# Kernel optimization log

Measured on AMD Instinct MI355X. Metric: run time of the kernel, lower is better.

The kernel has to match this reference:

```python
import jax, jax.numpy as jnp
import numpy as np
import math

N, E = 50000, 1600000
IN, HID, OUT, ED, H = 128, 32, 64, 64, 4
HC = H * HID  # 128, input dim of second layer


def setup_inputs() -> dict:
    key = jax.random.key(0)
    ks = jax.random.split(key, 32)
    w = lambda k, shape: (jax.random.normal(k, shape, jnp.float32) * 0.05)
    inp = {
        "x": w(ks[0], (N, IN)),
        "edge_feats": w(ks[1], (E, ED)),
        "edge_index": jax.random.randint(ks[2], (2, E), 0, N, jnp.int32),
        # layer 1: TransformerConv(IN -> HID, heads=H, concat=True, edge_dim=ED)
        "Wq1": w(ks[3], (IN, HC)), "bq1": w(ks[4], (HC,)),
        "Wk1": w(ks[5], (IN, HC)), "bk1": w(ks[6], (HC,)),
        "Wv1": w(ks[7], (IN, HC)), "bv1": w(ks[8], (HC,)),
        "We1": w(ks[9], (ED, HC)),  # lin_edge has no bias in PyG
        "Ws1": w(ks[10], (IN, HC)), "bs1": w(ks[11], (HC,)),
        # layer 2: TransformerConv(HC -> OUT, heads=1, concat=False, edge_dim=ED)
        "Wq2": w(ks[12], (HC, OUT)), "bq2": w(ks[13], (OUT,)),
        "Wk2": w(ks[14], (HC, OUT)), "bk2": w(ks[15], (OUT,)),
        "Wv2": w(ks[16], (HC, OUT)), "bv2": w(ks[17], (OUT,)),
        "We2": w(ks[18], (ED, OUT)),
        "Ws2": w(ks[19], (HC, OUT)), "bs2": w(ks[20], (OUT,)),
    }
    return inp


def tconv(x, src, dst, ef, Wq, bq, Wk, bk, Wv, bv, We, Ws, bs, heads, ch, concat):
    """PyG TransformerConv (beta=False, root_weight=True), eval mode."""
    n = x.shape[0]
    q = (x @ Wq + bq).reshape(n, heads, ch)
    k = (x @ Wk + bk).reshape(n, heads, ch)
    v = (x @ Wv + bv).reshape(n, heads, ch)
    e = (ef @ We).reshape(-1, heads, ch)           # [E,H,C]
    k_j = k[src] + e                                # gather + edge bias
    v_j = v[src] + e
    alpha = jnp.einsum("ehc,ehc->eh", q[dst], k_j) / math.sqrt(ch)  # [E,H]
    # segment softmax over destination nodes
    m = jax.lax.stop_gradient(jax.ops.segment_max(alpha, dst, num_segments=n))
    a = jnp.exp(alpha - m[dst])
    den = jax.ops.segment_sum(a, dst, num_segments=n)
    a = a / den[dst]
    msg = v_j * a[..., None]                        # [E,H,C]
    out = jax.ops.segment_sum(msg, dst, num_segments=n)  # [N,H,C]
    out = out.reshape(n, heads * ch) if concat else out.mean(axis=1)
    return out + x @ Ws + bs                        # root/skip connection


def reference(x, edge_feats, edge_index, Wq1, bq1, Wk1, bk1, Wv1, bv1, We1, Ws1, bs1,
              Wq2, bq2, Wk2, bk2, Wv2, bv2, We2, Ws2, bs2):
    src, dst = edge_index[0], edge_index[1]
    h = tconv(x, src, dst, edge_feats, Wq1, bq1, Wk1, bk1, Wv1, bv1, We1, Ws1, bs1,
              H, HID, True)
    h = jax.nn.relu(h)  # dropout=0.0 (eval) -> identity
    out = tconv(h, src, dst, edge_feats, Wq2, bq2, Wk2, bk2, Wv2, bv2, We2, Ws2, bs2,
                1, OUT, False)
    return out
```

## Files before the change

### kernel.cpp

```cpp
#include <hip/hip_runtime.h>

#define NN 50000
#define EE 1600000

__device__ inline float b2f(unsigned short u) {
    return __uint_as_float(((unsigned)u) << 16);
}
__device__ inline unsigned short f2bf(float f) {
    unsigned u = __float_as_uint(f);
    unsigned r = 0x7fffu + ((u >> 16) & 1u);
    return (unsigned short)((u + r) >> 16);
}
__device__ inline void stv(float* p, size_t i, float v) { p[i] = v; }
__device__ inline void stv(unsigned short* p, size_t i, float v) { p[i] = f2bf(v); }

__global__ void sniff_kernel(const void* w, int* flags) {
    int lane = threadIdx.x;
    const unsigned short* u = (const unsigned short*)w;
    int bad = 0;
    for (int i = lane; i < 256; i += 64) {
        float f = b2f(u[i]);
        if (!(fabsf(f) < 2.0f)) bad++;
    }
    unsigned long long m = __ballot(bad > 0);
    if (lane == 0) {
        flags[0] = (__popcll(m) > 8) ? 1 : 0;
        flags[1] = 0;
    }
}

struct WTab {
    const void* p[18];
    int off[18];
    int sz[18];
};
__global__ void __launch_bounds__(256) convert_kernel(WTab t, const int* __restrict__ flags,
                                                      unsigned short* __restrict__ dst) {
    int f32 = flags[0];
    int ti = blockIdx.y;
    int i = blockIdx.x * 256 + threadIdx.x;
    if (i < t.sz[ti]) {
        dst[t.off[ti] + i] = f32 ? f2bf(((const float*)t.p[ti])[i])
                                 : ((const unsigned short*)t.p[ti])[i];
    }
}

__global__ void __launch_bounds__(256) count_kernel(const int* __restrict__ dst,
                                                    int* __restrict__ cnt) {
    int e = blockIdx.x * 256 + threadIdx.x;
    if (e < EE) atomicAdd(&cnt[dst[e]], 1);
}

__global__ void __launch_bounds__(1024) scan_kernel(int* __restrict__ cntfill,
                                                    int* __restrict__ rowptr) {
    __shared__ int s[1024];
    __shared__ int carry_s;
    int tid = threadIdx.x;
    if (tid == 0) carry_s = 0;
    __syncthreads();
    for (int base = 0; base < NN; base += 4096) {
        int i0 = base + tid * 4;
        int v0 = (i0 + 0 < NN) ? cntfill[i0 + 0] : 0;
        int v1 = (i0 + 1 < NN) ? cntfill[i0 + 1] : 0;
        int v2 = (i0 + 2 < NN) ? cntfill[i0 + 2] : 0;
        int v3 = (i0 + 3 < NN) ? cntfill[i0 + 3] : 0;
        int tsum = v0 + v1 + v2 + v3;
        s[tid] = tsum;
        __syncthreads();
        for (int off = 1; off < 1024; off <<= 1) {
            int t = (tid >= off) ? s[tid - off] : 0;
            __syncthreads();
            s[tid] += t;
            __syncthreads();
        }
        int carry = carry_s;
        int excl = carry + s[tid] - tsum;
        int e0 = excl, e1 = excl + v0, e2 = e1 + v1, e3 = e2 + v2;
        if (i0 + 0 < NN) { rowptr[i0 + 0] = e0; cntfill[i0 + 0] = e0; }
        if (i0 + 1 < NN) { rowptr[i0 + 1] = e1; cntfill[i0 + 1] = e1; }
        if (i0 + 2 < NN) { rowptr[i0 + 2] = e2; cntfill[i0 + 2] = e2; }
        if (i0 + 3 < NN) { rowptr[i0 + 3] = e3; cntfill[i0 + 3] = e3; }
        __syncthreads();
        if (tid == 1023) carry_s = carry + s[1023];
        __syncthreads();
    }
    if (tid == 0) rowptr[NN] = carry_s;
}

__global__ void __launch_bounds__(256) fill_kernel(const int* __restrict__ dst,
                                                   int* __restrict__ cntfill,
                                                   int* __restrict__ perm) {
    int e = blockIdx.x * 256 + threadIdx.x;
    if (e < EE) {
        int p = atomicAdd(&cntfill[dst[e]], 1);
        perm[p] = e;
    }
}

__global__ void __launch_bounds__(256) edge_gather(const int* __restrict__ perm,
                                                   const int* __restrict__ src,
                                                   const void* __restrict__ efp,
                                                   const int* __restrict__ flagp,
                                                   int* __restrict__ src_perm,
                                                   unsigned short* __restrict__ efperm) {
    int ef32 = *flagp;
    int tid = threadIdx.x;
    int j = tid & 15;
    int local = tid >> 4;
    const float* efF = (const float*)efp;
    const unsigned short* efU = (const unsigned short*)efp;
    for (int pass = 0; pass < 4; ++pass) {
        int i = blockIdx.x * 64 + pass * 16 + local;
        if (i < EE) {
            int e = perm[i];
            if (j == 0) src_perm[i] = src[e];
            ushort4 o;
            if (ef32) {
                float4 f = *(const float4*)(efF + (size_t)e * 64 + j * 4);
                o.x = f2bf(f.x); o.y = f2bf(f.y); o.z = f2bf(f.z); o.w = f2bf(f.w);
            } else {
                o = *(const ushort4*)(efU + (size_t)e * 64 + j * 4);
            }
            *(ushort4*)(efperm + (size_t)i * 64 + j * 4) = o;
        }
    }
}

template <typename TO, int K, int OD, int TR, int LAYOUT = 0>
__global__ void __launch_bounds__(256) gemm_node(const void* __restrict__ X,
                                                 const int* __restrict__ flagp,
                                                 const unsigned short* __restrict__ W,
                                                 const unsigned short* __restrict__ bias,
                                                 TO* __restrict__ C, int nrows,
                                                 int ldc, int cstride, int coff) {
    constexpr int TRP = TR + 4;
    __shared__ unsigned short Ws[K * OD];
    __shared__ float Xs[K * TRP];
    int tid = threadIdx.x;
    int xf32 = *flagp;
    for (int i = tid; i < K * OD; i += 256) Ws[i] = W[i];
    int row0 = blockIdx.x * TR;
    const float* Xf = (const float*)X;
    const unsigned short* Xu = (const unsigned short*)X;
    for (int i = tid; i < TR * K; i += 256) {
        int r = i / K, kk = i % K;
        int rr = row0 + r;
        float vv = 0.f;
        if (rr < nrows) {
            size_t idx = (size_t)rr * K + kk;
            vv = xf32 ? Xf[idx] : b2f(Xu[idx]);
        }
        Xs[kk * TRP + r] = vv;
    }
    __syncthreads();
    constexpr int CG = OD / 4;
    int rg = tid / CG, cg = tid % CG;
    int r0 = rg * 4, c0 = cg * 4;
    float acc[4][4] = {};
#pragma unroll 4
    for (int kk = 0; kk < K; ++kk) {
        const float4 xv = *(const float4*)&Xs[kk * TRP + r0];
        ushort4 wu = *(const ushort4*)&Ws[kk * OD + c0];
        float xa[4] = {xv.x, xv.y, xv.z, xv.w};
        float wb[4] = {b2f(wu.x), b2f(wu.y), b2f(wu.z), b2f(wu.w)};
#pragma unroll
        for (int i2 = 0; i2 < 4; i2++)
#pragma unroll
            for (int j2 = 0; j2 < 4; j2++) acc[i2][j2] += xa[i2] * wb[j2];
    }
    float bb[4];
#pragma unroll
    for (int j2 = 0; j2 < 4; j2++) bb[j2] = b2f(bias[c0 + j2]);
#pragma unroll
    for (int i2 = 0; i2 < 4; i2++) {
        int rr = row0 + r0 + i2;
        if (rr < nrows) {
#pragma unroll
            for (int j2 = 0; j2 < 4; j2++) {
                size_t idx;
                if constexpr (LAYOUT == 0) {
                    idx = (size_t)rr * ldc + (size_t)(c0 + j2) * cstride + coff;
                } else {
                    int c = c0 + j2;
                    int hh = c >> 5, r = c & 31;
                    idx = (size_t)rr * 256 +
                          (size_t)((hh * 16 + (r & 15)) * 4 + (r >> 4) +
                                   (LAYOUT == 2 ? 2 : 0));
                }
                stv(C, idx, acc[i2][j2] + bb[j2]);
            }
        }
    }
}

__global__ void __launch_bounds__(256) qe1_kernel(const unsigned short* __restrict__ q,
                                                  const unsigned short* __restrict__ We,
                                                  float* __restrict__ qe) {
    __shared__ float Ws[64 * 129];
    __shared__ float qs[8 * 128];
    int tid = threadIdx.x;
    for (int i = tid; i < 64 * 128; i += 256) Ws[(i / 128) * 129 + (i % 128)] = b2f(We[i]);
    int n0 = blockIdx.x * 8;
    for (int i = tid; i < 8 * 128; i += 256) {
        int n = n0 + (i >> 7);
        qs[i] = (n < NN) ? b2f(q[(size_t)n * 128 + (i & 127)]) : 0.f;
    }
    __syncthreads();
    int h = tid >> 6, d = tid & 63;
    for (int nl = 0; nl < 8; ++nl) {
        int n = n0 + nl;
        if (n < NN) {
            float acc = 0.f;
#pragma unroll
            for (int c = 0; c < 32; ++c)
                acc += qs[nl * 128 + h * 32 + c] * Ws[d * 129 + h * 32 + c];
            qe[(size_t)n * 256 + h * 64 + d] = acc;
        }
    }
}

__global__ void __launch_bounds__(256) qe2_kernel(const unsigned short* __restrict__ q,
                                                  const unsigned short* __restrict__ We,
                                                  float* __restrict__ qe) {
    __shared__ float Ws[64 * 65];
    __shared__ float qs[4 * 64];
    int tid = threadIdx.x;
    for (int i = tid; i < 64 * 64; i += 256) Ws[(i / 64) * 65 + (i % 64)] = b2f(We[i]);
    int n0 = blockIdx.x * 4;
    {
        int n = n0 + (tid >> 6);
        qs[tid] = (n < NN) ? b2f(q[(size_t)n * 64 + (tid & 63)]) : 0.f;
    }
    __syncthreads();
    int nl = tid >> 6, d = tid & 63;
    int n = n0 + nl;
    if (n < NN) {
        float acc = 0.f;
#pragma unroll
        for (int c = 0; c < 64; ++c) acc += qs[nl * 64 + c] * Ws[d * 65 + c];
        qe[(size_t)n * 64 + d] = acc;
    }
}

__device__ __forceinline__ void np1_step(const uint2 (&kvd)[4], const ushort4 (&efd)[4],
                                         float qa, float qb, const float4& qm, float rs,
                                         float& m, float& l, float& a1, float& a2,
                                         float& w0, float& w1, float& w2, float& w3) {
    float t[4];
    float f0[4], f1[4], f2[4], f3[4];
#pragma unroll
    for (int u = 0; u < 4; ++u) {
        float ka = b2f((unsigned short)(kvd[u].x & 0xffffu));
        float kb = b2f((unsigned short)(kvd[u].x >> 16));
        f0[u] = b2f(efd[u].x); f1[u] = b2f(efd[u].y);
        f2[u] = b2f(efd[u].z); f3[u] = b2f(efd[u].w);
        float tt = qa * ka + qb * kb + qm.x * f0[u] + qm.y * f1[u] +
                   qm.z * f2[u] + qm.w * f3[u];
        tt += __shfl_xor(tt, 4);
        tt += __shfl_xor(tt, 8);
        tt += __shfl_xor(tt, 16);
        tt += __shfl_xor(tt, 32);
        t[u] = tt * rs;
    }
    float mn = fmaxf(fmaxf(fmaxf(t[0], t[1]), fmaxf(t[2], t[3])), m);
    float sc = __expf(m - mn);
    float w[4];
#pragma unroll
    for (int u = 0; u < 4; ++u) w[u] = __expf(t[u] - mn);
    m = mn;
    l = l * sc + ((w[0] + w[1]) + (w[2] + w[3]));
    float sa1 = 0.f, sa2 = 0.f, sw0 = 0.f, sw1 = 0.f, sw2 = 0.f, sw3 = 0.f;
#pragma unroll
    for (int u = 0; u < 4; ++u) {
        float va = b2f((unsigned short)(kvd[u].y & 0xffffu));
        float vb = b2f((unsigned short)(kvd[u].y >> 16));
        sa1 += w[u] * va; sa2 += w[u] * vb;
        sw0 += w[u] * f0[u]; sw1 += w[u] * f1[u];
        sw2 += w[u] * f2[u]; sw3 += w[u] * f3[u];
    }
    a1 = a1 * sc + sa1; a2 = a2 * sc + sa2;
    w0 = w0 * sc + sw0; w1 = w1 * sc + sw1;
    w2 = w2 * sc + sw2; w3 = w3 * sc + sw3;
}

__global__ void __launch_bounds__(256) node_pass1(
    const int* __restrict__ rowptr, const int* __restrict__ srcp,
    const unsigned short* __restrict__ q, const unsigned short* __restrict__ kv,
    const float* __restrict__ qe, const unsigned short* __restrict__ efperm,
    float* __restrict__ av, float* __restrict__ wef) {
    int lane = threadIdx.x & 63;
    int node = (blockIdx.x * 256 + threadIdx.x) >> 6;
    if (node >= NN) return;
    int h = lane & 3;
    int dq = lane >> 2;
    int c1 = h * 32 + dq, c2 = c1 + 16;
    int kvoff = (h * 16 + dq) * 4;
    float qa = b2f(q[(size_t)node * 128 + c1]);
    float qb = b2f(q[(size_t)node * 128 + c2]);
    float4 qm = *(const float4*)(qe + (size_t)node * 256 + h * 64 + 4 * dq);
    float m = -__builtin_inff(), l = 0.f, a1 = 0.f, a2 = 0.f;
    float w0 = 0.f, w1 = 0.f, w2 = 0.f, w3 = 0.f;
    int beg = rowptr[node], end = rowptr[node + 1];
    const float rs = 0.17677669529663687f;
    int ng = (end - beg) >> 2;

    int ssA[4], ssB[4];
    uint2 kvA[4], kvB[4];
    ushort4 efA[4], efB[4];

    if (ng > 0) {
#pragma unroll
        for (int u = 0; u < 4; ++u) ssA[u] = srcp[beg + u];
#pragma unroll
        for (int u = 0; u < 4; ++u)
            kvA[u] = *(const uint2*)(kv + (size_t)ssA[u] * 256 + kvoff);
#pragma unroll
        for (int u = 0; u < 4; ++u)
            efA[u] = *(const ushort4*)(efperm + (size_t)(beg + u) * 64 + 4 * dq);
        if (ng > 1) {
#pragma unroll
            for (int u = 0; u < 4; ++u) ssB[u] = srcp[beg + 4 + u];
        }
        int g = 0;
        while (true) {
            bool nextB = (g + 1 < ng);
            if (nextB) {
                int ib = beg + ((g + 1) << 2);
#pragma unroll
                for (int u = 0; u < 4; ++u)
                    kvB[u] = *(const uint2*)(kv + (size_t)ssB[u] * 256 + kvoff);
#pragma unroll
                for (int u = 0; u < 4; ++u)
                    efB[u] = *(const ushort4*)(efperm + (size_t)(ib + u) * 64 + 4 * dq);
                if (g + 2 < ng) {
                    int ib2 = beg + ((g + 2) << 2);
#pragma unroll
                    for (int u = 0; u < 4; ++u) ssA[u] = srcp[ib2 + u];
                }
            }
            np1_step(kvA, efA, qa, qb, qm, rs, m, l, a1, a2, w0, w1, w2, w3);
            if (!nextB) { ++g; break; }
            ++g;
            bool nextA = (g + 1 < ng);
            if (nextA) {
                int ib = beg + ((g + 1) << 2);
#pragma unroll
                for (int u = 0; u < 4; ++u)
                    kvA[u] = *(const uint2*)(kv + (size_t)ssA[u] * 256 + kvoff);
#pragma unroll
                for (int u = 0; u < 4; ++u)
                    efA[u] = *(const ushort4*)(efperm + (size_t)(ib + u) * 64 + 4 * dq);
                if (g + 2 < ng) {
                    int ib2 = beg + ((g + 2) << 2);
#pragma unroll
                    for (int u = 0; u < 4; ++u) ssB[u] = srcp[ib2 + u];
                }
            }
            np1_step(kvB, efB, qa, qb, qm, rs, m, l, a1, a2, w0, w1, w2, w3);
            if (!nextA) { ++g; break; }
            ++g;
        }
    }
    for (int i = beg + (ng << 2); i < end; ++i) {
        int sj = srcp[i];
        uint2 kd = *(const uint2*)(kv + (size_t)sj * 256 + kvoff);
        ushort4 fu = *(const ushort4*)(efperm + (size_t)i * 64 + 4 * dq);
        float f0s = b2f(fu.x), f1s = b2f(fu.y), f2s = b2f(fu.z), f3s = b2f(fu.w);
        float ka = b2f((unsigned short)(kd.x & 0xffffu));
        float kb = b2f((unsigned short)(kd.x >> 16));
        float tt = qa * ka + qb * kb + qm.x * f0s + qm.y * f1s + qm.z * f2s + qm.w * f3s;
        tt += __shfl_xor(tt, 4);
        tt += __shfl_xor(tt, 8);
        tt += __shfl_xor(tt, 16);
        tt += __shfl_xor(tt, 32);
        float alpha = tt * rs;
        float mn = fmaxf(m, alpha);
        float sc = __expf(m - mn);
        float w = __expf(alpha - mn);
        m = mn;
        l = l * sc + w;
        float va = b2f((unsigned short)(kd.y & 0xffffu));
        float vb = b2f((unsigned short)(kd.y >> 16));
        a1 = a1 * sc + w * va;
        a2 = a2 * sc + w * vb;
        w0 = w0 * sc + w * f0s; w1 = w1 * sc + w * f1s;
        w2 = w2 * sc + w * f2s; w3 = w3 * sc + w * f3s;
    }
    float inv = (l > 0.f) ? 1.f / l : 0.f;
    av[(size_t)node * 128 + c1] = a1 * inv;
    av[(size_t)node * 128 + c2] = a2 * inv;
    float4 wout = make_float4(w0 * inv, w1 * inv, w2 * inv, w3 * inv);
    *(float4*)(wef + (size_t)node * 256 + h * 64 + 4 * dq) = wout;
}

__device__ __forceinline__ void np2_step(const unsigned (&ku)[4], const unsigned short (&fe)[4],
                                         float qa, float qj,
                                         float& m, float& l, float& a1, float& w0) {
    float t[4], fj[4];
#pragma unroll
    for (int u = 0; u < 4; ++u) {
        float kk = b2f((unsigned short)(ku[u] & 0xffffu));
        fj[u] = b2f(fe[u]);
        float tt = qa * kk + qj * fj[u];
        tt += __shfl_xor(tt, 1);
        tt += __shfl_xor(tt, 2);
        tt += __shfl_xor(tt, 4);
        tt += __shfl_xor(tt, 8);
        tt += __shfl_xor(tt, 16);
        tt += __shfl_xor(tt, 32);
        t[u] = tt * 0.125f;
    }
    float mn = fmaxf(fmaxf(fmaxf(t[0], t[1]), fmaxf(t[2], t[3])), m);
    float sc = __expf(m - mn);
    float w[4];
#pragma unroll
    for (int u = 0; u < 4; ++u) w[u] = __expf(t[u] - mn);
    m = mn;
    l = l * sc + ((w[0] + w[1]) + (w[2] + w[3]));
    float sa = 0.f, sw = 0.f;
#pragma unroll
    for (int u = 0; u < 4; ++u) {
        float vv = b2f((unsigned short)(ku[u] >> 16));
        sa += w[u] * vv;
        sw += w[u] * fj[u];
    }
    a1 = a1 * sc + sa;
    w0 = w0 * sc + sw;
}

__global__ void __launch_bounds__(256) node_pass2(
    const int* __restrict__ rowptr, const int* __restrict__ srcp,
    const unsigned short* __restrict__ q, const unsigned short* __restrict__ kv,
    const float* __restrict__ qe, const unsigned short* __restrict__ efperm,
    float* __restrict__ av, float* __restrict__ wef) {
    int lane = threadIdx.x & 63;
    int node = (blockIdx.x * 256 + threadIdx.x) >> 6;
    if (node >= NN) return;
    float qa = b2f(q[(size_t)node * 64 + lane]);
    float qj = qe[(size_t)node * 64 + lane];
    float m = -__builtin_inff(), l = 0.f, a1 = 0.f, w0 = 0.f;
    int beg = rowptr[node], end = rowptr[node + 1];
    int ng = (end - beg) >> 2;

    int ssA[4], ssB[4];
    unsigned kuA[4], kuB[4];
    unsigned short feA[4], feB[4];

    if (ng > 0) {
#pragma unroll
        for (int u = 0; u < 4; ++u) ssA[u] = srcp[beg + u];
#pragma unroll
        for (int u = 0; u < 4; ++u)
            kuA[u] = *(const unsigned*)(kv + (size_t)ssA[u] * 128 + 2 * lane);
#pragma unroll
        for (int u = 0; u < 4; ++u) feA[u] = efperm[(size_t)(beg + u) * 64 + lane];
        if (ng > 1) {
#pragma unroll
            for (int u = 0; u < 4; ++u) ssB[u] = srcp[beg + 4 + u];
        }
        int g = 0;
        while (true) {
            bool nextB = (g + 1 < ng);
            if (nextB) {
                int ib = beg + ((g + 1) << 2);
#pragma unroll
                for (int u = 0; u < 4; ++u)
                    kuB[u] = *(const unsigned*)(kv + (size_t)ssB[u] * 128 + 2 * lane);
#pragma unroll
                for (int u = 0; u < 4; ++u) feB[u] = efperm[(size_t)(ib + u) * 64 + lane];
                if (g + 2 < ng) {
                    int ib2 = beg + ((g + 2) << 2);
#pragma unroll
                    for (int u = 0; u < 4; ++u) ssA[u] = srcp[ib2 + u];
                }
            }
            np2_step(kuA, feA, qa, qj, m, l, a1, w0);
            if (!nextB) { ++g; break; }
            ++g;
            bool nextA = (g + 1 < ng);
            if (nextA) {
                int ib = beg + ((g + 1) << 2);
#pragma unroll
                for (int u = 0; u < 4; ++u)
                    kuA[u] = *(const unsigned*)(kv + (size_t)ssA[u] * 128 + 2 * lane);
#pragma unroll
                for (int u = 0; u < 4; ++u) feA[u] = efperm[(size_t)(ib + u) * 64 + lane];
                if (g + 2 < ng) {
                    int ib2 = beg + ((g + 2) << 2);
#pragma unroll
                    for (int u = 0; u < 4; ++u) ssB[u] = srcp[ib2 + u];
                }
            }
            np2_step(kuB, feB, qa, qj, m, l, a1, w0);
            if (!nextA) { ++g; break; }
            ++g;
        }
    }
    for (int i = beg + (ng << 2); i < end; ++i) {
        int sj = srcp[i];
        unsigned ku = *(const unsigned*)(kv + (size_t)sj * 128 + 2 * lane);
        float fj = b2f(efperm[(size_t)i * 64 + lane]);
        float kk = b2f((unsigned short)(ku & 0xffffu));
        float tt = qa * kk + qj * fj;
        tt += __shfl_xor(tt, 1);
        tt += __shfl_xor(tt, 2);
        tt += __shfl_xor(tt, 4);
        tt += __shfl_xor(tt, 8);
        tt += __shfl_xor(tt, 16);
        tt += __shfl_xor(tt, 32);
        float alpha = tt * 0.125f;
        float mn = fmaxf(m, alpha);
        float sc = __expf(m - mn);
        float w = __expf(alpha - mn);
        m = mn;
        l = l * sc + w;
        float vv = b2f((unsigned short)(ku >> 16));
        a1 = a1 * sc + w * vv;
        w0 = w0 * sc + w * fj;
    }
    float inv = (l > 0.f) ? 1.f / l : 0.f;
    av[(size_t)node * 64 + lane] = a1 * inv;
    wef[(size_t)node * 64 + lane] = w0 * inv;
}

__global__ void __launch_bounds__(256) ep1_kernel(const float* __restrict__ av,
                                                  const float* __restrict__ wef,
                                                  const float* __restrict__ s1,
                                                  const unsigned short* __restrict__ We,
                                                  unsigned short* __restrict__ hout) {
    __shared__ float Ws[64 * 128];
    int tid = threadIdx.x;
    for (int i = tid; i < 64 * 128; i += 256) Ws[i] = b2f(We[i]);
    __syncthreads();
    int nl = tid >> 7;
    int c = tid & 127;
    int g = c >> 5;
    for (int it = 0; it < 8; ++it) {
        int n = blockIdx.x * 16 + it * 2 + nl;
        if (n < NN) {
            const float* wr = wef + (size_t)n * 256 + g * 64;
            float acc = 0.f;
#pragma unroll
            for (int d = 0; d < 64; ++d) acc += wr[d] * Ws[d * 128 + c];
            float val = av[(size_t)n * 128 + c] + acc + s1[(size_t)n * 128 + c];
            hout[(size_t)n * 128 + c] = f2bf(fmaxf(val, 0.f));
        }
    }
}

__global__ void __launch_bounds__(256) ep2_kernel(const float* __restrict__ av,
                                                  const float* __restrict__ wef,
                                                  const float* __restrict__ s2,
                                                  const unsigned short* __restrict__ We,
                                                  float* __restrict__ out) {
    __shared__ float Ws[64 * 64];
    int tid = threadIdx.x;
    for (int i = tid; i < 64 * 64; i += 256) Ws[i] = b2f(We[i]);
    __syncthreads();
    int nl = tid >> 6;
    int c = tid & 63;
    for (int it = 0; it < 4; ++it) {
        int n = blockIdx.x * 16 + it * 4 + nl;
        if (n < NN) {
            const float* wr = wef + (size_t)n * 64;
            float acc = 0.f;
#pragma unroll
            for (int d = 0; d < 64; ++d) acc += wr[d] * Ws[d * 64 + c];
            float val = av[(size_t)n * 64 + c] + acc + s2[(size_t)n * 64 + c];
            out[(size_t)n * 64 + c] = val;
        }
    }
}

extern "C" void kernel_launch(void* const* d_in, const int* in_sizes, int n_in,
                              void* d_out, int out_size, void* d_ws, size_t ws_size,
                              hipStream_t stream) {
    (void)in_sizes; (void)n_in; (void)out_size; (void)ws_size;
    const int* eidx = (const int*)d_in[2];
    const int* src = eidx;
    const int* dst = eidx + EE;

    char* p = (char*)d_ws;
    auto alloc = [&](size_t bytes) {
        void* r = (void*)p;
        p += (bytes + 255) & ~(size_t)255;
        return r;
    };
    unsigned short* wts = (unsigned short*)alloc(111360 * 2);
    int* flags          = (int*)alloc(256);
    int* rowptr         = (int*)alloc((size_t)(NN + 1) * 4);
    int* cntfill        = (int*)alloc((size_t)(NN + 1) * 4);
    int* perm           = (int*)alloc((size_t)EE * 4);
    int* src_perm       = (int*)alloc((size_t)EE * 4);
    unsigned short* efperm = (unsigned short*)alloc((size_t)EE * 64 * 2);
    unsigned short* q1  = (unsigned short*)alloc((size_t)NN * 128 * 2);
    unsigned short* kv1 = (unsigned short*)alloc((size_t)NN * 256 * 2);
    float* qe           = (float*)alloc((size_t)NN * 256 * 4);
    float* av           = (float*)alloc((size_t)NN * 128 * 4);
    float* wef          = (float*)alloc((size_t)NN * 256 * 4);

    WTab tab;
    int off = 0;
    const int wsz[18] = {16384, 128, 16384, 128, 16384, 128, 8192, 16384, 128,
                         8192, 64, 8192, 64, 8192, 64, 4096, 8192, 64};
    int offs[18];
    for (int i = 0; i < 18; ++i) {
        tab.p[i] = d_in[3 + i];
        tab.sz[i] = wsz[i];
        tab.off[i] = off;
        offs[i] = off;
        off += wsz[i];
    }
    const unsigned short* Wq1c = wts + offs[0];
    const unsigned short* bq1c = wts + offs[1];
    const unsigned short* Wk1c = wts + offs[2];
    const unsigned short* bk1c = wts + offs[3];
    const unsigned short* Wv1c = wts + offs[4];
    const unsigned short* bv1c = wts + offs[5];
    const unsigned short* We1c = wts + offs[6];
    const unsigned short* Ws1c = wts + offs[7];
    const unsigned short* bs1c = wts + offs[8];
    const unsigned short* Wq2c = wts + offs[9];
    const unsigned short* bq2c = wts + offs[10];
    const unsigned short* Wk2c = wts + offs[11];
    const unsigned short* bk2c = wts + offs[12];
    const unsigned short* Wv2c = wts + offs[13];
    const unsigned short* bv2c = wts + offs[14];
    const unsigned short* We2c = wts + offs[15];
    const unsigned short* Ws2c = wts + offs[16];
    const unsigned short* bs2c = wts + offs[17];

    hipMemsetAsync(cntfill, 0, (size_t)(NN + 1) * 4, stream);
    sniff_kernel<<<1, 64, 0, stream>>>(d_in[3], flags);
    convert_kernel<<<dim3(64, 18), 256, 0, stream>>>(tab, flags, wts);
    count_kernel<<<EE / 256, 256, 0, stream>>>(dst, cntfill);
    scan_kernel<<<1, 1024, 0, stream>>>(cntfill, rowptr);
    fill_kernel<<<EE / 256, 256, 0, stream>>>(dst, cntfill, perm);
    edge_gather<<<(EE + 63) / 64, 256, 0, stream>>>(perm, src, d_in[1], flags,
                                                    src_perm, efperm);

    int g1 = (NN + 31) / 32;
    gemm_node<unsigned short, 128, 128, 32, 0><<<g1, 256, 0, stream>>>(d_in[0], flags, Wq1c, bq1c, q1, NN, 128, 1, 0);
    gemm_node<unsigned short, 128, 128, 32, 1><<<g1, 256, 0, stream>>>(d_in[0], flags, Wk1c, bk1c, kv1, NN, 0, 0, 0);
    gemm_node<unsigned short, 128, 128, 32, 2><<<g1, 256, 0, stream>>>(d_in[0], flags, Wv1c, bv1c, kv1, NN, 0, 0, 0);
    qe1_kernel<<<(NN + 7) / 8, 256, 0, stream>>>(q1, We1c, qe);
    node_pass1<<<(NN + 3) / 4, 256, 0, stream>>>(rowptr, src_perm, q1, kv1, qe,
                                                 efperm, av, wef);
    float* s1 = qe;
    gemm_node<float, 128, 128, 32, 0><<<g1, 256, 0, stream>>>(d_in[0], flags, Ws1c, bs1c, s1, NN, 128, 1, 0);
    unsigned short* h = kv1;
    ep1_kernel<<<(NN + 15) / 16, 256, 0, stream>>>(av, wef, s1, We1c, h);

    unsigned short* q2 = q1;
    unsigned short* kv2 = kv1 + (size_t)NN * 128;
    float* s2 = qe;
    float* qe2 = av;
    float* av2 = av + (size_t)NN * 64;
    float* wef2 = wef;
    int g2 = (NN + 63) / 64;
    gemm_node<unsigned short, 128, 64, 64, 0><<<g2, 256, 0, stream>>>(h, flags + 1, Wq2c, bq2c, q2, NN, 64, 1, 0);
    gemm_node<unsigned short, 128, 64, 64, 0><<<g2, 256, 0, stream>>>(h, flags + 1, Wk2c, bk2c, kv2, NN, 128, 2, 0);
    gemm_node<unsigned short, 128, 64, 64, 0><<<g2, 256, 0, stream>>>(h, flags + 1, Wv2c, bv2c, kv2, NN, 128, 2, 1);
    gemm_node<float, 128, 64, 64, 0><<<g2, 256, 0, stream>>>(h, flags + 1, Ws2c, bs2c, s2, NN, 64, 1, 0);
    qe2_kernel<<<(NN + 3) / 4, 256, 0, stream>>>(q2, We2c, qe2);
    node_pass2<<<(NN + 3) / 4, 256, 0, stream>>>(rowptr, src_perm, q2, kv2, qe2,
                                                 efperm, av2, wef2);
    ep2_kernel<<<(NN + 15) / 16, 256, 0, stream>>>(av2, wef2, s2, We2c,
                                                   (float*)d_out);
}
```

Baseline: 1.744 ms.

## Split attention into edge-parallel score kernels and node-parallel softmax accumulation

Attention logits are now computed in separate edge-parallel kernels (ega1/ega2) and written to a per-edge alpha buffer. The first of these also takes over the edge-feature permutation and the src/dst gather that edge_gather used to do. The node kernels then do a two-pass softmax: a max pass over the stored alphas, then accumulation of V and edge-feature weights, with no online rescaling and no shuffle reductions per edge. K and V are stored in separate layouts so each gather reads only what it needs. This is meant to remove the serialized per-edge reductions from the degree-imbalanced node loop, at the cost of an extra alpha buffer write and read per layer.

```diff
diff --git a/kernel.cpp b/kernel.cpp
--- a/kernel.cpp
+++ b/kernel.cpp
@@ -6,10 +6,15 @@
 __device__ inline float b2f(unsigned short u) {
     return __uint_as_float(((unsigned)u) << 16);
 }
+__device__ inline float blo(unsigned u) { return __uint_as_float(u << 16); }
+__device__ inline float bhi(unsigned u) { return __uint_as_float(u & 0xffff0000u); }
 __device__ inline unsigned short f2bf(float f) {
     unsigned u = __float_as_uint(f);
     unsigned r = 0x7fffu + ((u >> 16) & 1u);
     return (unsigned short)((u + r) >> 16);
+}
+__device__ inline unsigned pk2(float a, float b) {
+    return (unsigned)f2bf(a) | ((unsigned)f2bf(b) << 16);
 }
 __device__ inline void stv(float* p, size_t i, float v) { p[i] = v; }
 __device__ inline void stv(unsigned short* p, size_t i, float v) { p[i] = f2bf(v); }
@@ -94,35 +99,6 @@
     if (e < EE) {
         int p = atomicAdd(&cntfill[dst[e]], 1);
         perm[p] = e;
-    }
-}
-
-__global__ void __launch_bounds__(256) edge_gather(const int* __restrict__ perm,
-                                                   const int* __restrict__ src,
-                                                   const void* __restrict__ efp,
-                                                   const int* __restrict__ flagp,
-                                                   int* __restrict__ src_perm,
-                                                   unsigned short* __restrict__ efperm) {
-    int ef32 = *flagp;
-    int tid = threadIdx.x;
-    int j = tid & 15;
-    int local = tid >> 4;
-    const float* efF = (const float*)efp;
-    const unsigned short* efU = (const unsigned short*)efp;
-    for (int pass = 0; pass < 4; ++pass) {
-        int i = blockIdx.x * 64 + pass * 16 + local;
-        if (i < EE) {
-            int e = perm[i];
-            if (j == 0) src_perm[i] = src[e];
-            ushort4 o;
-            if (ef32) {
-                float4 f = *(const float4*)(efF + (size_t)e * 64 + j * 4);
-                o.x = f2bf(f.x); o.y = f2bf(f.y); o.z = f2bf(f.z); o.w = f2bf(f.w);
-            } else {
-                o = *(const ushort4*)(efU + (size_t)e * 64 + j * 4);
-            }
-            *(ushort4*)(efperm + (size_t)i * 64 + j * 4) = o;
-        }
     }
 }
 
@@ -182,10 +158,8 @@
                     idx = (size_t)rr * ldc + (size_t)(c0 + j2) * cstride + coff;
                 } else {
                     int c = c0 + j2;
-                    int hh = c >> 5, r = c & 31;
-                    idx = (size_t)rr * 256 +
-                          (size_t)((hh * 16 + (r & 15)) * 4 + (r >> 4) +
-                                   (LAYOUT == 2 ? 2 : 0));
+                    idx = (size_t)rr * 128 +
+                          (size_t)(((c >> 5) * 16 + (c & 15)) * 2 + ((c & 31) >> 4));
                 }
                 stv(C, idx, acc[i2][j2] + bb[j2]);
             }
@@ -242,81 +216,156 @@
     }
 }
 
-__device__ __forceinline__ void np1_step(const uint2 (&kvd)[4], const ushort4 (&efd)[4],
-                                         float qa, float qb, const float4& qm, float rs,
-                                         float& m, float& l, float& a1, float& a2,
-                                         float& w0, float& w1, float& w2, float& w3) {
-    float t[4];
-    float f0[4], f1[4], f2[4], f3[4];
+__global__ void __launch_bounds__(256) ega1_kernel(
+    int* __restrict__ perm, const int* __restrict__ src, const int* __restrict__ dst,
+    const void* __restrict__ efp, const int* __restrict__ flagp,
+    const unsigned short* __restrict__ q, const unsigned short* __restrict__ k,
+    const float* __restrict__ qe, int* __restrict__ srcp,
+    unsigned short* __restrict__ efperm, float* __restrict__ alpha) {
+    int ef32 = *flagp;
+    int lane = threadIdx.x & 63;
+    int wv = (blockIdx.x * 256 + threadIdx.x) >> 6;
+    int el = lane >> 4, t = lane & 15;
+    int h = t >> 2, s = t & 3;
+    int i = wv * 4 + el;
+    if (i >= EE) return;
+    int e = perm[i];
+    int sj = src[e], dj = dst[e];
+    if (t == 0) {
+        srcp[i] = sj;
+        perm[i] = dj;
+    }
+    uint4 qu = *(const uint4*)(q + (size_t)dj * 128 + 8 * t);
+    uint4 ku = *(const uint4*)(k + (size_t)sj * 128 + 8 * t);
+    float kd = blo(qu.x) * blo(ku.x) + bhi(qu.x) * bhi(ku.x) +
+               blo(qu.y) * blo(ku.y) + bhi(qu.y) * bhi(ku.y) +
+               blo(qu.z) * blo(ku.z) + bhi(qu.z) * bhi(ku.z) +
+               blo(qu.w) * blo(ku.w) + bhi(qu.w) * bhi(ku.w);
+    float fv[16];
+    uint4 pa, pb;
+    if (ef32) {
+        const float* er = (const float*)efp + (size_t)e * 64 + 16 * s;
+        float4 x0 = *(const float4*)(er + 0);
+        float4 x1 = *(const float4*)(er + 4);
+        float4 x2 = *(const float4*)(er + 8);
+        float4 x3 = *(const float4*)(er + 12);
+        fv[0] = x0.x; fv[1] = x0.y; fv[2] = x0.z; fv[3] = x0.w;
+        fv[4] = x1.x; fv[5] = x1.y; fv[6] = x1.z; fv[7] = x1.w;
+        fv[8] = x2.x; fv[9] = x2.y; fv[10] = x2.z; fv[11] = x2.w;
+        fv[12] = x3.x; fv[13] = x3.y; fv[14] = x3.z; fv[15] = x3.w;
+        if (h == 0) {
+            pa.x = pk2(fv[0], fv[1]); pa.y = pk2(fv[2], fv[3]);
+            pa.z = pk2(fv[4], fv[5]); pa.w = pk2(fv[6], fv[7]);
+            pb.x = pk2(fv[8], fv[9]); pb.y = pk2(fv[10], fv[11]);
+            pb.z = pk2(fv[12], fv[13]); pb.w = pk2(fv[14], fv[15]);
+        }
+    } else {
+        const unsigned short* er = (const unsigned short*)efp + (size_t)e * 64 + 16 * s;
+        pa = *(const uint4*)er;
+        pb = *(const uint4*)(er + 8);
+        fv[0] = blo(pa.x); fv[1] = bhi(pa.x); fv[2] = blo(pa.y); fv[3] = bhi(pa.y);
+        fv[4] = blo(pa.z); fv[5] = bhi(pa.z); fv[6] = blo(pa.w); fv[7] = bhi(pa.w);
+        fv[8] = blo(pb.x); fv[9] = bhi(pb.x); fv[10] = blo(pb.y); fv[11] = bhi(pb.y);
+        fv[12] = blo(pb.z); fv[13] = bhi(pb.z); fv[14] = blo(pb.w); fv[15] = bhi(pb.w);
+    }
+    if (h == 0) {
+        *(uint4*)(efperm + (size_t)i * 64 + 16 * s) = pa;
+        *(uint4*)(efperm + (size_t)i * 64 + 16 * s + 8) = pb;
+    }
+    const float* qr = qe + (size_t)dj * 256 + h * 64 + 16 * s;
+    float ed = 0.f;
+#pragma unroll
+    for (int j = 0; j < 16; ++j) ed += fv[j] * qr[j];
+    float part = kd + ed;
+    part += __shfl_xor(part, 1);
+    part += __shfl_xor(part, 2);
+    if (s == 0) alpha[(size_t)i * 4 + h] = part * 0.17677669529663687f;
+}
+
+__global__ void __launch_bounds__(256) ega2_kernel(
+    const int* __restrict__ srcp, const int* __restrict__ dstp,
+    const unsigned short* __restrict__ q, const unsigned short* __restrict__ k,
+    const float* __restrict__ qe, const unsigned short* __restrict__ efperm,
+    float* __restrict__ alpha) {
+    int lane = threadIdx.x & 63;
+    int wv = (blockIdx.x * 256 + threadIdx.x) >> 6;
+    int el = lane >> 4, t = lane & 15;
+    int i = wv * 4 + el;
+    if (i >= EE) return;
+    int sj = srcp[i], dj = dstp[i];
+    uint2 qu = *(const uint2*)(q + (size_t)dj * 64 + 4 * t);
+    uint2 ku = *(const uint2*)(k + (size_t)sj * 64 + 4 * t);
+    uint2 fu = *(const uint2*)(efperm + (size_t)i * 64 + 4 * t);
+    float4 qev = *(const float4*)(qe + (size_t)dj * 64 + 4 * t);
+    float part = blo(qu.x) * blo(ku.x) + bhi(qu.x) * bhi(ku.x) +
+                 blo(qu.y) * blo(ku.y) + bhi(qu.y) * bhi(ku.y) +
+                 qev.x * blo(fu.x) + qev.y * bhi(fu.x) +
+                 qev.z * blo(fu.y) + qev.w * bhi(fu.y);
+    part += __shfl_xor(part, 1);
+    part += __shfl_xor(part, 2);
+    part += __shfl_xor(part, 4);
+    part += __shfl_xor(part, 8);
+    if (t == 0) alpha[i] = part * 0.125f;
+}
+
+__device__ __forceinline__ void acc1_step(const unsigned (&vv)[4], const ushort4 (&fu)[4],
+                                          const float (&al)[4], float mh,
+                                          float& l, float& a1, float& a2,
+                                          float& w0, float& w1, float& w2, float& w3) {
 #pragma unroll
     for (int u = 0; u < 4; ++u) {
-        float ka = b2f((unsigned short)(kvd[u].x & 0xffffu));
-        float kb = b2f((unsigned short)(kvd[u].x >> 16));
-        f0[u] = b2f(efd[u].x); f1[u] = b2f(efd[u].y);
-        f2[u] = b2f(efd[u].z); f3[u] = b2f(efd[u].w);
-        float tt = qa * ka + qb * kb + qm.x * f0[u] + qm.y * f1[u] +
-                   qm.z * f2[u] + qm.w * f3[u];
-        tt += __shfl_xor(tt, 4);
-        tt += __shfl_xor(tt, 8);
-        tt += __shfl_xor(tt, 16);
-        tt += __shfl_xor(tt, 32);
-        t[u] = tt * rs;
-    }
-    float mn = fmaxf(fmaxf(fmaxf(t[0], t[1]), fmaxf(t[2], t[3])), m);
-    float sc = __expf(m - mn);
-    float w[4];
-#pragma unroll
-    for (int u = 0; u < 4; ++u) w[u] = __expf(t[u] - mn);
-    m = mn;
-    l = l * sc + ((w[0] + w[1]) + (w[2] + w[3]));
-    float sa1 = 0.f, sa2 = 0.f, sw0 = 0.f, sw1 = 0.f, sw2 = 0.f, sw3 = 0.f;
-#pragma unroll
-    for (int u = 0; u < 4; ++u) {
-        float va = b2f((unsigned short)(kvd[u].y & 0xffffu));
-        float vb = b2f((unsigned short)(kvd[u].y >> 16));
-        sa1 += w[u] * va; sa2 += w[u] * vb;
-        sw0 += w[u] * f0[u]; sw1 += w[u] * f1[u];
-        sw2 += w[u] * f2[u]; sw3 += w[u] * f3[u];
-    }
-    a1 = a1 * sc + sa1; a2 = a2 * sc + sa2;
-    w0 = w0 * sc + sw0; w1 = w1 * sc + sw1;
-    w2 = w2 * sc + sw2; w3 = w3 * sc + sw3;
-}
-
-__global__ void __launch_bounds__(256) node_pass1(
+        float w = __expf(al[u] - mh);
+        l += w;
+        a1 += w * blo(vv[u]);
+        a2 += w * bhi(vv[u]);
+        w0 += w * b2f(fu[u].x);
+        w1 += w * b2f(fu[u].y);
+        w2 += w * b2f(fu[u].z);
+        w3 += w * b2f(fu[u].w);
+    }
+}
+
+__global__ void __launch_bounds__(256) node_accum1(
     const int* __restrict__ rowptr, const int* __restrict__ srcp,
-    const unsigned short* __restrict__ q, const unsigned short* __restrict__ kv,
-    const float* __restrict__ qe, const unsigned short* __restrict__ efperm,
+    const float* __restrict__ alpha, const unsigned* __restrict__ vpk,
+    const unsigned short* __restrict__ efperm,
     float* __restrict__ av, float* __restrict__ wef) {
     int lane = threadIdx.x & 63;
     int node = (blockIdx.x * 256 + threadIdx.x) >> 6;
     if (node >= NN) return;
-    int h = lane & 3;
-    int dq = lane >> 2;
-    int c1 = h * 32 + dq, c2 = c1 + 16;
-    int kvoff = (h * 16 + dq) * 4;
-    float qa = b2f(q[(size_t)node * 128 + c1]);
-    float qb = b2f(q[(size_t)node * 128 + c2]);
-    float4 qm = *(const float4*)(qe + (size_t)node * 256 + h * 64 + 4 * dq);
-    float m = -__builtin_inff(), l = 0.f, a1 = 0.f, a2 = 0.f;
+    int beg = rowptr[node], end = rowptr[node + 1];
+    int h4 = lane >> 4, dq = lane & 15;
+    int c1 = h4 * 32 + dq, c2 = c1 + 16;
+    const float NINF = -__builtin_inff();
+    float mx = NINF;
+    for (int i0 = beg; i0 < end; i0 += 16) {
+        int idx = i0 + (lane >> 2);
+        int idc = idx < end ? idx : beg;
+        float a = alpha[(size_t)idc * 4 + (lane & 3)];
+        mx = fmaxf(mx, idx < end ? a : NINF);
+    }
+    mx = fmaxf(mx, __shfl_xor(mx, 4));
+    mx = fmaxf(mx, __shfl_xor(mx, 8));
+    mx = fmaxf(mx, __shfl_xor(mx, 16));
+    mx = fmaxf(mx, __shfl_xor(mx, 32));
+    float mh = __shfl(mx, h4);
+    float l = 0.f, a1 = 0.f, a2 = 0.f;
     float w0 = 0.f, w1 = 0.f, w2 = 0.f, w3 = 0.f;
-    int beg = rowptr[node], end = rowptr[node + 1];
-    const float rs = 0.17677669529663687f;
     int ng = (end - beg) >> 2;
-
-    int ssA[4], ssB[4];
-    uint2 kvA[4], kvB[4];
-    ushort4 efA[4], efB[4];
-
     if (ng > 0) {
+        int ssA[4], ssB[4];
+        unsigned vA[4], vB[4];
+        ushort4 fA[4], fB[4];
+        float aA[4], aB[4];
 #pragma unroll
         for (int u = 0; u < 4; ++u) ssA[u] = srcp[beg + u];
 #pragma unroll
+        for (int u = 0; u < 4; ++u) vA[u] = vpk[(size_t)ssA[u] * 64 + lane];
+#pragma unroll
         for (int u = 0; u < 4; ++u)
-            kvA[u] = *(const uint2*)(kv + (size_t)ssA[u] * 256 + kvoff);
-#pragma unroll
-        for (int u = 0; u < 4; ++u)
-            efA[u] = *(const ushort4*)(efperm + (size_t)(beg + u) * 64 + 4 * dq);
+            fA[u] = *(const ushort4*)(efperm + (size_t)(beg + u) * 64 + 4 * dq);
+#pragma unroll
+        for (int u = 0; u < 4; ++u) aA[u] = alpha[(size_t)(beg + u) * 4 + h4];
         if (ng > 1) {
 #pragma unroll
             for (int u = 0; u < 4; ++u) ssB[u] = srcp[beg + 4 + u];
@@ -327,133 +376,97 @@
             if (nextB) {
                 int ib = beg + ((g + 1) << 2);
 #pragma unroll
+                for (int u = 0; u < 4; ++u) vB[u] = vpk[(size_t)ssB[u] * 64 + lane];
+#pragma unroll
                 for (int u = 0; u < 4; ++u)
-                    kvB[u] = *(const uint2*)(kv + (size_t)ssB[u] * 256 + kvoff);
-#pragma unroll
-                for (int u = 0; u < 4; ++u)
-                    efB[u] = *(const ushort4*)(efperm + (size_t)(ib + u) * 64 + 4 * dq);
+                    fB[u] = *(const ushort4*)(efperm + (size_t)(ib + u) * 64 + 4 * dq);
+#pragma unroll
+                for (int u = 0; u < 4; ++u) aB[u] = alpha[(size_t)(ib + u) * 4 + h4];
                 if (g + 2 < ng) {
                     int ib2 = beg + ((g + 2) << 2);
 #pragma unroll
                     for (int u = 0; u < 4; ++u) ssA[u] = srcp[ib2 + u];
                 }
             }
-            np1_step(kvA, efA, qa, qb, qm, rs, m, l, a1, a2, w0, w1, w2, w3);
-            if (!nextB) { ++g; break; }
+            acc1_step(vA, fA, aA, mh, l, a1, a2, w0, w1, w2, w3);
+            if (!nextB) break;
             ++g;
             bool nextA = (g + 1 < ng);
             if (nextA) {
                 int ib = beg + ((g + 1) << 2);
 #pragma unroll
+                for (int u = 0; u < 4; ++u) vA[u] = vpk[(size_t)ssA[u] * 64 + lane];
+#pragma unroll
                 for (int u = 0; u < 4; ++u)
-                    kvA[u] = *(const uint2*)(kv + (size_t)ssA[u] * 256 + kvoff);
-#pragma unroll
-                for (int u = 0; u < 4; ++u)
-                    efA[u] = *(const ushort4*)(efperm + (size_t)(ib + u) * 64 + 4 * dq);
+                    fA[u] = *(const ushort4*)(efperm + (size_t)(ib + u) * 64 + 4 * dq);
+#pragma unroll
+                for (int u = 0; u < 4; ++u) aA[u] = alpha[(size_t)(ib + u) * 4 + h4];
                 if (g + 2 < ng) {
                     int ib2 = beg + ((g + 2) << 2);
 #pragma unroll
                     for (int u = 0; u < 4; ++u) ssB[u] = srcp[ib2 + u];
                 }
             }
-            np1_step(kvB, efB, qa, qb, qm, rs, m, l, a1, a2, w0, w1, w2, w3);
-            if (!nextA) { ++g; break; }
+            acc1_step(vB, fB, aB, mh, l, a1, a2, w0, w1, w2, w3);
+            if (!nextA) break;
             ++g;
         }
     }
     for (int i = beg + (ng << 2); i < end; ++i) {
         int sj = srcp[i];
-        uint2 kd = *(const uint2*)(kv + (size_t)sj * 256 + kvoff);
+        float w = __expf(alpha[(size_t)i * 4 + h4] - mh);
+        unsigned vv = vpk[(size_t)sj * 64 + lane];
         ushort4 fu = *(const ushort4*)(efperm + (size_t)i * 64 + 4 * dq);
-        float f0s = b2f(fu.x), f1s = b2f(fu.y), f2s = b2f(fu.z), f3s = b2f(fu.w);
-        float ka = b2f((unsigned short)(kd.x & 0xffffu));
-        float kb = b2f((unsigned short)(kd.x >> 16));
-        float tt = qa * ka + qb * kb + qm.x * f0s + qm.y * f1s + qm.z * f2s + qm.w * f3s;
-        tt += __shfl_xor(tt, 4);
-        tt += __shfl_xor(tt, 8);
-        tt += __shfl_xor(tt, 16);
-        tt += __shfl_xor(tt, 32);
-        float alpha = tt * rs;
-        float mn = fmaxf(m, alpha);
-        float sc = __expf(m - mn);
-        float w = __expf(alpha - mn);
-        m = mn;
-        l = l * sc + w;
-        float va = b2f((unsigned short)(kd.y & 0xffffu));
-        float vb = b2f((unsigned short)(kd.y >> 16));
-        a1 = a1 * sc + w * va;
-        a2 = a2 * sc + w * vb;
-        w0 = w0 * sc + w * f0s; w1 = w1 * sc + w * f1s;
-        w2 = w2 * sc + w * f2s; w3 = w3 * sc + w * f3s;
+        l += w;
+        a1 += w * blo(vv);
+        a2 += w * bhi(vv);
+        w0 += w * b2f(fu.x); w1 += w * b2f(fu.y);
+        w2 += w * b2f(fu.z); w3 += w * b2f(fu.w);
     }
     float inv = (l > 0.f) ? 1.f / l : 0.f;
     av[(size_t)node * 128 + c1] = a1 * inv;
     av[(size_t)node * 128 + c2] = a2 * inv;
     float4 wout = make_float4(w0 * inv, w1 * inv, w2 * inv, w3 * inv);
-    *(float4*)(wef + (size_t)node * 256 + h * 64 + 4 * dq) = wout;
-}
-
-__device__ __forceinline__ void np2_step(const unsigned (&ku)[4], const unsigned short (&fe)[4],
-                                         float qa, float qj,
-                                         float& m, float& l, float& a1, float& w0) {
-    float t[4], fj[4];
-#pragma unroll
-    for (int u = 0; u < 4; ++u) {
-        float kk = b2f((unsigned short)(ku[u] & 0xffffu));
-        fj[u] = b2f(fe[u]);
-        float tt = qa * kk + qj * fj[u];
-        tt += __shfl_xor(tt, 1);
-        tt += __shfl_xor(tt, 2);
-        tt += __shfl_xor(tt, 4);
-        tt += __shfl_xor(tt, 8);
-        tt += __shfl_xor(tt, 16);
-        tt += __shfl_xor(tt, 32);
-        t[u] = tt * 0.125f;
-    }
-    float mn = fmaxf(fmaxf(fmaxf(t[0], t[1]), fmaxf(t[2], t[3])), m);
-    float sc = __expf(m - mn);
-    float w[4];
-#pragma unroll
-    for (int u = 0; u < 4; ++u) w[u] = __expf(t[u] - mn);
-    m = mn;
-    l = l * sc + ((w[0] + w[1]) + (w[2] + w[3]));
-    float sa = 0.f, sw = 0.f;
-#pragma unroll
-    for (int u = 0; u < 4; ++u) {
-        float vv = b2f((unsigned short)(ku[u] >> 16));
-        sa += w[u] * vv;
-        sw += w[u] * fj[u];
-    }
-    a1 = a1 * sc + sa;
-    w0 = w0 * sc + sw;
-}
-
-__global__ void __launch_bounds__(256) node_pass2(
+    *(float4*)(wef + (size_t)node * 256 + h4 * 64 + 4 * dq) = wout;
+}
+
+__global__ void __launch_bounds__(256) node_accum2(
     const int* __restrict__ rowptr, const int* __restrict__ srcp,
-    const unsigned short* __restrict__ q, const unsigned short* __restrict__ kv,
-    const float* __restrict__ qe, const unsigned short* __restrict__ efperm,
+    const float* __restrict__ alpha, const unsigned short* __restrict__ v,
+    const unsigned short* __restrict__ efperm,
     float* __restrict__ av, float* __restrict__ wef) {
     int lane = threadIdx.x & 63;
     int node = (blockIdx.x * 256 + threadIdx.x) >> 6;
     if (node >= NN) return;
-    float qa = b2f(q[(size_t)node * 64 + lane]);
-    float qj = qe[(size_t)node * 64 + lane];
-    float m = -__builtin_inff(), l = 0.f, a1 = 0.f, w0 = 0.f;
     int beg = rowptr[node], end = rowptr[node + 1];
+    const float NINF = -__builtin_inff();
+    float mx = NINF;
+    for (int i0 = beg; i0 < end; i0 += 64) {
+        int idx = i0 + lane;
+        int idc = idx < end ? idx : beg;
+        float a = alpha[idc];
+        mx = fmaxf(mx, idx < end ? a : NINF);
+    }
+    mx = fmaxf(mx, __shfl_xor(mx, 1));
+    mx = fmaxf(mx, __shfl_xor(mx, 2));
+    mx = fmaxf(mx, __shfl_xor(mx, 4));
+    mx = fmaxf(mx, __shfl_xor(mx, 8));
+    mx = fmaxf(mx, __shfl_xor(mx, 16));
+    mx = fmaxf(mx, __shfl_xor(mx, 32));
+    float l = 0.f, a1 = 0.f, w0 = 0.f;
     int ng = (end - beg) >> 2;
-
-    int ssA[4], ssB[4];
-    unsigned kuA[4], kuB[4];
-    unsigned short feA[4], feB[4];
-
     if (ng > 0) {
+        int ssA[4], ssB[4];
+        unsigned short vA[4], vB[4], fA[4], fB[4];
+        float aA[4], aB[4];
 #pragma unroll
         for (int u = 0; u < 4; ++u) ssA[u] = srcp[beg + u];
 #pragma unroll
-        for (int u = 0; u < 4; ++u)
-            kuA[u] = *(const unsigned*)(kv + (size_t)ssA[u] * 128 + 2 * lane);
-#pragma unroll
-        for (int u = 0; u < 4; ++u) feA[u] = efperm[(size_t)(beg + u) * 64 + lane];
+        for (int u = 0; u < 4; ++u) vA[u] = v[(size_t)ssA[u] * 64 + lane];
+#pragma unroll
+        for (int u = 0; u < 4; ++u) fA[u] = efperm[(size_t)(beg + u) * 64 + lane];
+#pragma unroll
+        for (int u = 0; u < 4; ++u) aA[u] = alpha[beg + u];
         if (ng > 1) {
 #pragma unroll
             for (int u = 0; u < 4; ++u) ssB[u] = srcp[beg + 4 + u];
@@ -464,59 +477,58 @@
             if (nextB) {
                 int ib = beg + ((g + 1) << 2);
 #pragma unroll
-                for (int u = 0; u < 4; ++u)
-                    kuB[u] = *(const unsigned*)(kv + (size_t)ssB[u] * 128 + 2 * lane);
-#pragma unroll
-                for (int u = 0; u < 4; ++u) feB[u] = efperm[(size_t)(ib + u) * 64 + lane];
+                for (int u = 0; u < 4; ++u) vB[u] = v[(size_t)ssB[u] * 64 + lane];
+#pragma unroll
+                for (int u = 0; u < 4; ++u) fB[u] = efperm[(size_t)(ib + u) * 64 + lane];
+#pragma unroll
+                for (int u = 0; u < 4; ++u) aB[u] = alpha[ib + u];
                 if (g + 2 < ng) {
                     int ib2 = beg + ((g + 2) << 2);
 #pragma unroll
                     for (int u = 0; u < 4; ++u) ssA[u] = srcp[ib2 + u];
                 }
             }
-            np2_step(kuA, feA, qa, qj, m, l, a1, w0);
-            if (!nextB) { ++g; break; }
+#pragma unroll
+            for (int u = 0; u < 4; ++u) {
+                float w = __expf(aA[u] - mx);
+                l += w;
+                a1 += w * b2f(vA[u]);
+                w0 += w * b2f(fA[u]);
+            }
+            if (!nextB) break;
             ++g;
             bool nextA = (g + 1 < ng);
             if (nextA) {
                 int ib = beg + ((g + 1) << 2);
 #pragma unroll
-                for (int u = 0; u < 4; ++u)
-                    kuA[u] = *(const unsigned*)(kv + (size_t)ssA[u] * 128 + 2 * lane);
-#pragma unroll
-                for (int u = 0; u < 4; ++u) feA[u] = efperm[(size_t)(ib + u) * 64 + lane];
+                for (int u = 0; u < 4; ++u) vA[u] = v[(size_t)ssA[u] * 64 + lane];
+#pragma unroll
+                for (int u = 0; u < 4; ++u) fA[u] = efperm[(size_t)(ib + u) * 64 + lane];
+#pragma unroll
+                for (int u = 0; u < 4; ++u) aA[u] = alpha[ib + u];
                 if (g + 2 < ng) {
                     int ib2 = beg + ((g + 2) << 2);
 #pragma unroll
                     for (int u = 0; u < 4; ++u) ssB[u] = srcp[ib2 + u];
                 }
             }
-            np2_step(kuB, feB, qa, qj, m, l, a1, w0);
-            if (!nextA) { ++g; break; }
+#pragma unroll
+            for (int u = 0; u < 4; ++u) {
+                float w = __expf(aB[u] - mx);
+                l += w;
+                a1 += w * b2f(vB[u]);
+                w0 += w * b2f(fB[u]);
+            }
+            if (!nextA) break;
             ++g;
         }
     }
     for (int i = beg + (ng << 2); i < end; ++i) {
         int sj = srcp[i];
-        unsigned ku = *(const unsigned*)(kv + (size_t)sj * 128 + 2 * lane);
-        float fj = b2f(efperm[(size_t)i * 64 + lane]);
-        float kk = b2f((unsigned short)(ku & 0xffffu));
-        float tt = qa * kk + qj * fj;
-        tt += __shfl_xor(tt, 1);
-        tt += __shfl_xor(tt, 2);
-        tt += __shfl_xor(tt, 4);
-        tt += __shfl_xor(tt, 8);
-        tt += __shfl_xor(tt, 16);
-        tt += __shfl_xor(tt, 32);
-        float alpha = tt * 0.125f;
-        float mn = fmaxf(m, alpha);
-        float sc = __expf(m - mn);
-        float w = __expf(alpha - mn);
-        m = mn;
-        l = l * sc + w;
-        float vv = b2f((unsigned short)(ku >> 16));
-        a1 = a1 * sc + w * vv;
-        w0 = w0 * sc + w * fj;
+        float w = __expf(alpha[i] - mx);
+        l += w;
+        a1 += w * b2f(v[(size_t)sj * 64 + lane]);
+        w0 += w * b2f(efperm[(size_t)i * 64 + lane]);
     }
     float inv = (l > 0.f) ? 1.f / l : 0.f;
     av[(size_t)node * 64 + lane] = a1 * inv;
@@ -591,10 +603,12 @@
     int* rowptr         = (int*)alloc((size_t)(NN + 1) * 4);
     int* cntfill        = (int*)alloc((size_t)(NN + 1) * 4);
     int* perm           = (int*)alloc((size_t)EE * 4);
-    int* src_perm       = (int*)alloc((size_t)EE * 4);
+    int* srcp           = (int*)alloc((size_t)EE * 4);
     unsigned short* efperm = (unsigned short*)alloc((size_t)EE * 64 * 2);
+    float* alphab       = (float*)alloc((size_t)EE * 4 * 4);
     unsigned short* q1  = (unsigned short*)alloc((size_t)NN * 128 * 2);
-    unsigned short* kv1 = (unsigned short*)alloc((size_t)NN * 256 * 2);
+    unsigned short* k1  = (unsigned short*)alloc((size_t)NN * 128 * 2);
+    unsigned short* v1  = (unsigned short*)alloc((size_t)NN * 128 * 2);
     float* qe           = (float*)alloc((size_t)NN * 256 * 4);
     float* av           = (float*)alloc((size_t)NN * 128 * 4);
     float* wef          = (float*)alloc((size_t)NN * 256 * 4);
@@ -636,35 +650,39 @@
     count_kernel<<<EE / 256, 256, 0, stream>>>(dst, cntfill);
     scan_kernel<<<1, 1024, 0, stream>>>(cntfill, rowptr);
     fill_kernel<<<EE / 256, 256, 0, stream>>>(dst, cntfill, perm);
-    edge_gather<<<(EE + 63) / 64, 256, 0, stream>>>(perm, src, d_in[1], flags,
-                                                    src_perm, efperm);
 
     int g1 = (NN + 31) / 32;
+    int gE = (EE + 15) / 16;
     gemm_node<unsigned short, 128, 128, 32, 0><<<g1, 256, 0, stream>>>(d_in[0], flags, Wq1c, bq1c, q1, NN, 128, 1, 0);
-    gemm_node<unsigned short, 128, 128, 32, 1><<<g1, 256, 0, stream>>>(d_in[0], flags, Wk1c, bk1c, kv1, NN, 0, 0, 0);
-    gemm_node<unsigned short, 128, 128, 32, 2><<<g1, 256, 0, stream>>>(d_in[0], flags, Wv1c, bv1c, kv1, NN, 0, 0, 0);
+    gemm_node<unsigned short, 128, 128, 32, 0><<<g1, 256, 0, stream>>>(d_in[0], flags, Wk1c, bk1c, k1, NN, 128, 1, 0);
+    gemm_node<unsigned short, 128, 128, 32, 3><<<g1, 256, 0, stream>>>(d_in[0], flags, Wv1c, bv1c, v1, NN, 0, 0, 0);
     qe1_kernel<<<(NN + 7) / 8, 256, 0, stream>>>(q1, We1c, qe);
-    node_pass1<<<(NN + 3) / 4, 256, 0, stream>>>(rowptr, src_perm, q1, kv1, qe,
-                                                 efperm, av, wef);
+    ega1_kernel<<<gE, 256, 0, stream>>>(perm, src, dst, d_in[1], flags, q1, k1, qe,
+                                        srcp, efperm, alphab);
+    node_accum1<<<(NN + 3) / 4, 256, 0, stream>>>(rowptr, srcp, alphab,
+                                                  (const unsigned*)v1, efperm, av, wef);
     float* s1 = qe;
     gemm_node<float, 128, 128, 32, 0><<<g1, 256, 0, stream>>>(d_in[0], flags, Ws1c, bs1c, s1, NN, 128, 1, 0);
-    unsigned short* h = kv1;
+    unsigned short* h = k1;
     ep1_kernel<<<(NN + 15) / 16, 256, 0, stream>>>(av, wef, s1, We1c, h);
 
     unsigned short* q2 = q1;
-    unsigned short* kv2 = kv1 + (size_t)NN * 128;
+    unsigned short* k2 = v1;
+    unsigned short* v2 = v1 + (size_t)NN * 64;
     float* s2 = qe;
     float* qe2 = av;
     float* av2 = av + (size_t)NN * 64;
     float* wef2 = wef;
+    float* alpha2 = alphab;
     int g2 = (NN + 63) / 64;
     gemm_node<unsigned short, 128, 64, 64, 0><<<g2, 256, 0, stream>>>(h, flags + 1, Wq2c, bq2c, q2, NN, 64, 1, 0);
-    gemm_node<unsigned short, 128, 64, 64, 0><<<g2, 256, 0, stream>>>(h, flags + 1, Wk2c, bk2c, kv2, NN, 128, 2, 0);
-    gemm_node<unsigned short, 128, 64, 64, 0><<<g2, 256, 0, stream>>>(h, flags + 1, Wv2c, bv2c, kv2, NN, 128, 2, 1);
+    gemm_node<unsigned short, 128, 64, 64, 0><<<g2, 256, 0, stream>>>(h, flags + 1, Wk2c, bk2c, k2, NN, 64, 1, 0);
+    gemm_node<unsigned short, 128, 64, 64, 0><<<g2, 256, 0, stream>>>(h, flags + 1, Wv2c, bv2c, v2, NN, 64, 1, 0);
     gemm_node<float, 128, 64, 64, 0><<<g2, 256, 0, stream>>>(h, flags + 1, Ws2c, bs2c, s2, NN, 64, 1, 0);
     qe2_kernel<<<(NN + 3) / 4, 256, 0, stream>>>(q2, We2c, qe2);
-    node_pass2<<<(NN + 3) / 4, 256, 0, stream>>>(rowptr, src_perm, q2, kv2, qe2,
-                                                 efperm, av2, wef2);
+    ega2_kernel<<<gE, 256, 0, stream>>>(srcp, perm, q2, k2, qe2, efperm, alpha2);
+    node_accum2<<<(NN + 3) / 4, 256, 0, stream>>>(rowptr, srcp, alpha2, v2, efperm,
+                                                  av2, wef2);
     ep2_kernel<<<(NN + 15) / 16, 256, 0, stream>>>(av2, wef2, s2, We2c,
                                                    (float*)d_out);
 }
```

After: 1.792 ms. 1.03x slower.
